# Optimization experiments

Hardware: AMD Instinct MI355X
Metric: run time of the kernel (lower is better)

Reference implementation:

```python
import jax, jax.numpy as jnp
import numpy as np
import math

B, S, D, H = 4, 2048, 1024, 16
HD = D // H
WINDOW = 86400.0 * 7.0  # 7 days, per create_time_mask(window_size=...)


def setup_inputs() -> dict:
    key = jax.random.key(0)
    ks = jax.random.split(key, 12)
    x = jax.random.normal(ks[0], (B, S, D), dtype=jnp.float32)
    # transaction timestamps: uniform over 30 days, sorted per sequence
    timestamps = jnp.sort(jax.random.uniform(ks[1], (B, S), dtype=jnp.float32) * (86400.0 * 30.0), axis=-1)
    init = 0.02
    Wq = jax.random.normal(ks[2], (D, D), dtype=jnp.float32) * init
    bq = jnp.zeros((D,), dtype=jnp.float32)
    Wk = jax.random.normal(ks[3], (D, D), dtype=jnp.float32) * init
    bk = jnp.zeros((D,), dtype=jnp.float32)
    Wv = jax.random.normal(ks[4], (D, D), dtype=jnp.float32) * init
    bv = jnp.zeros((D,), dtype=jnp.float32)
    Wo = jax.random.normal(ks[5], (D, D), dtype=jnp.float32) * init
    bo = jnp.zeros((D,), dtype=jnp.float32)
    Wc = jax.random.normal(ks[6], (1, D), dtype=jnp.float32) * init
    bc = jnp.zeros((1,), dtype=jnp.float32)
    return {"x": x, "timestamps": timestamps, "Wq": Wq, "bq": bq, "Wk": Wk, "bk": bk,
            "Wv": Wv, "bv": bv, "Wo": Wo, "bo": bo, "Wc": Wc, "bc": bc}


def reference(x, timestamps, Wq, bq, Wk, bk, Wv, bv, Wo, bo, Wc, bc):
    b, s, d = x.shape
    scale = 1.0 / math.sqrt(HD)
    # projections (torch Linear: y = x @ W.T + b), split heads -> [b, s, H, HD]
    Q = (x @ Wq.T + bq).reshape(b, s, H, HD)
    K = (x @ Wk.T + bk).reshape(b, s, H, HD)
    V = (x @ Wv.T + bv).reshape(b, s, H, HD)
    # scores [b, H, q, k]
    scores = jnp.einsum('bqhd,bkhd->bhqk', Q, K) * scale
    # time-window mask: attend only within +/- WINDOW seconds
    time_mask = jnp.abs(timestamps[:, :, None] - timestamps[:, None, :]) <= WINDOW  # [b, s, s]
    scores = jnp.where(time_mask[:, None, :, :], scores, -jnp.inf)
    attn = jax.nn.softmax(scores, axis=-1)
    attended = jnp.einsum('bhqk,bkhd->bqhd', attn, V).reshape(b, s, d)
    output = attended @ Wo.T + bo
    change_scores = (output @ Wc.T + bc)[..., 0]  # [b, s]
    return output, change_scores
```

## Files before the change

### kernel.cpp

```cpp
#include <hip/hip_runtime.h>
#include <math.h>

#define BB 4
#define SS 2048
#define DD 1024
#define HH 16
#define HDD 64
#define NN (BB*SS)
#define WINDOWF 604800.0f
#define LOG2E 1.44269504088896340736f
#define SCALE2 (0.125f * LOG2E)

typedef __attribute__((ext_vector_type(8))) short bf16x8;
typedef __attribute__((ext_vector_type(4))) short bf16x4;
typedef __attribute__((ext_vector_type(4))) short s16x4;
typedef __attribute__((ext_vector_type(4))) float f32x4;

__device__ __forceinline__ unsigned short f2b(float f) {
    unsigned int x = __float_as_uint(f);
    unsigned int r = x + 0x7FFFu + ((x >> 16) & 1u);
    return (unsigned short)(r >> 16);
}

__device__ __forceinline__ unsigned int cvt_pk_bf16(float lo, float hi) {
    unsigned int r;
    asm("v_cvt_pk_bf16_f32 %0, %1, %2" : "=v"(r) : "v"(lo), "v"(hi));
    return r;
}

__device__ __forceinline__ void gload16(const unsigned short* g, unsigned short* l) {
    __builtin_amdgcn_global_load_lds(
        (const __attribute__((address_space(1))) unsigned int*)g,
        (__attribute__((address_space(3))) unsigned int*)l, 16, 0, 0);
}

__global__ __launch_bounds__(256)
void cvt_band(const float* __restrict__ x,
              const float* __restrict__ Wq, const float* __restrict__ Wk,
              const float* __restrict__ Wv, const float* __restrict__ Wo,
              const float* __restrict__ ts,
              unsigned short* __restrict__ xb,
              unsigned short* __restrict__ Wqb, unsigned short* __restrict__ Wkb,
              unsigned short* __restrict__ Wvb, unsigned short* __restrict__ Wob,
              int* __restrict__ lo, int* __restrict__ hi)
{
    const int g = blockIdx.x;
    const int tid = threadIdx.x;
    if (g < 12288) {
        const float* src; unsigned short* dst; int i;
        if (g < 8192) { src = x; dst = xb; i = g * 1024 + tid * 4; }
        else {
            const int wi = (g - 8192) >> 10;
            src = (wi == 0) ? Wq : (wi == 1) ? Wk : (wi == 2) ? Wv : Wo;
            dst = (wi == 0) ? Wqb : (wi == 1) ? Wkb : (wi == 2) ? Wvb : Wob;
            i = ((g - 8192) & 1023) * 1024 + tid * 4;
        }
        float4 v = *(const float4*)(src + i);
        s16x4 o;
        o[0] = (short)f2b(v.x); o[1] = (short)f2b(v.y);
        o[2] = (short)f2b(v.z); o[3] = (short)f2b(v.w);
        *(s16x4*)(dst + i) = o;
    } else {
        const int idx = (g - 12288) * 256 + tid;
        const int b = idx / SS, q = idx % SS;
        const float* t = ts + (size_t)b * SS;
        float tq = t[q];
        float lot = tq - WINDOWF - 1.0f;
        float hit = tq + WINDOWF + 1.0f;
        int l = 0, r = q;
        while (l < r) { int m = (l + r) >> 1; if (t[m] < lot) l = m + 1; else r = m; }
        lo[idx] = l;
        int l2 = q, r2 = SS - 1;
        while (l2 < r2) { int m = (l2 + r2 + 1) >> 1; if (t[m] > hit) r2 = m - 1; else l2 = m; }
        hi[idx] = l2;
    }
}

template<int OUTMODE>
__global__ __launch_bounds__(256)
void gemm_bf16(const unsigned short* __restrict__ A,
               const unsigned short* __restrict__ Bw,
               const float* __restrict__ bias,
               void* __restrict__ Y, int M, int N, int K, float alpha)
{
    constexpr int BM = 128, BN = 128, BK = 64;
    __shared__ unsigned short As[BM * BK];
    __shared__ unsigned short Bs[BN * BK];

    const int bm = blockIdx.x * BM;
    const int bn = blockIdx.y * BN;
    const int tid = threadIdx.x;
    const int wid = tid >> 6, l = tid & 63;
    const int wm = (wid >> 1) * 64, wn = (wid & 1) * 64;
    const int lr = l & 15, lg = l >> 4;

    const int srow = l >> 3;
    const int schunk = ((l & 7) ^ srow) * 8;

    f32x4 acc[4][4];
#pragma unroll
    for (int i = 0; i < 4; ++i)
#pragma unroll
        for (int j = 0; j < 4; ++j) acc[i][j] = (f32x4){0.f, 0.f, 0.f, 0.f};

    for (int k0 = 0; k0 < K; k0 += BK) {
#pragma unroll
        for (int i = 0; i < 4; ++i) {
            const int r0 = wid * 32 + i * 8;
            gload16(A  + (size_t)(bm + r0 + srow) * K + k0 + schunk, &As[r0 * BK]);
            gload16(Bw + (size_t)(bn + r0 + srow) * K + k0 + schunk, &Bs[r0 * BK]);
        }
        __syncthreads();

#pragma unroll
        for (int ks = 0; ks < 2; ++ks) {
            bf16x8 af[4], bf[4];
#pragma unroll
            for (int am = 0; am < 4; ++am) {
                const int row = wm + am * 16 + lr;
                af[am] = *(const bf16x8*)&As[row * BK + (((ks * 4 + lg) ^ (row & 7)) * 8)];
            }
#pragma unroll
            for (int nf = 0; nf < 4; ++nf) {
                const int row = wn + nf * 16 + lr;
                bf[nf] = *(const bf16x8*)&Bs[row * BK + (((ks * 4 + lg) ^ (row & 7)) * 8)];
            }
#pragma unroll
            for (int am = 0; am < 4; ++am)
#pragma unroll
                for (int nf = 0; nf < 4; ++nf)
                    acc[am][nf] = __builtin_amdgcn_mfma_f32_16x16x32_bf16(
                        af[am], bf[nf], acc[am][nf], 0, 0, 0);
        }
        __syncthreads();
    }

    float bia[4];
#pragma unroll
    for (int nf = 0; nf < 4; ++nf) bia[nf] = bias[bn + wn + nf * 16 + lr];

#pragma unroll
    for (int am = 0; am < 4; ++am)
#pragma unroll
        for (int nf = 0; nf < 4; ++nf) {
            if (OUTMODE == 2) {
                int mbase = bm + wm + am * 16 + lg * 4;
                int n = bn + wn + nf * 16 + lr;
                int bidx = mbase >> 11, sidx = mbase & (SS - 1);
                s16x4 o;
#pragma unroll
                for (int r = 0; r < 4; ++r)
                    o[r] = (short)f2b((acc[am][nf][r] + bia[nf]) * alpha);
                *(s16x4*)((unsigned short*)Y +
                          (((size_t)(bidx << 10) + n) << 11) + sidx) = o;
            } else {
#pragma unroll
                for (int r = 0; r < 4; ++r) {
                    float o = (acc[am][nf][r] + bia[nf]) * alpha;
                    size_t m = (size_t)(bm + wm + am * 16 + lg * 4 + r);
                    size_t n = (size_t)(bn + wn + nf * 16 + lr);
                    if (OUTMODE == 1) ((unsigned short*)Y)[m * N + n] = f2b(o);
                    else              ((float*)Y)[m * N + n] = o;
                }
            }
        }
}

__global__ __launch_bounds__(256)
void attn_mfma(const unsigned short* __restrict__ Qb, const unsigned short* __restrict__ Kb,
               const unsigned short* __restrict__ Vt, const float* __restrict__ Tg,
               const int* __restrict__ lo, const int* __restrict__ hi,
               unsigned short* __restrict__ Ab)
{
    __shared__ unsigned short Ks[2][64 * 64];
    __shared__ unsigned short Vs[2][64 * 64];

    const int blk = blockIdx.x;
    const int xcd = blk & 7;
    const int idx = blk >> 3;
    const int bh  = xcd * 8 + (idx >> 5);
    const int qt  = idx & 31;
    const int b = bh >> 4, h = bh & 15;

    const int tid = threadIdx.x;
    const int wid = tid >> 6, l = tid & 63;
    const int lr = l & 15, lg = l >> 4;
    const int q0w = qt * 64 + wid * 16;

    const size_t qrow = (size_t)(b * SS + q0w + lr);
    const bf16x8 qf0 = *(const bf16x8*)(Qb + qrow * DD + h * HDD + lg * 8);
    const bf16x8 qf1 = *(const bf16x8*)(Qb + qrow * DD + h * HDD + 32 + lg * 8);

    const float* tb = Tg + (size_t)b * SS;
    const float tq = tb[q0w + lr];
    const float tq_min = tb[qt * 64];
    const float tq_max = tb[qt * 64 + 63];

    const int t0 = lo[b * SS + qt * 64] >> 6;
    const int t1 = hi[b * SS + qt * 64 + 63] >> 6;

    const unsigned short* Kbh = Kb + (size_t)b * SS * DD + h * HDD;
    const unsigned short* Vth = Vt + ((size_t)(b * 1024 + h * HDD)) * SS;

    const int srow = l >> 3;
    const int schunk = ((l & 7) ^ srow) * 8;

    const unsigned short* kg0 = Kbh + (size_t)(t0 * 64 + wid * 16 + srow) * DD + schunk;
    const unsigned short* kg1 = kg0 + 8 * DD;
    const unsigned short* vg0 = Vth + (size_t)(wid * 16 + srow) * SS + t0 * 64 + schunk;
    const unsigned short* vg1 = vg0 + 8 * SS;

    const int x = lr & 7;
    const int ka_off = lr * 64 + ((lg ^ x) << 3);
    const int w = (lg & 1) * 4;
    const int pvA = lr * 64 + ((((lg >> 1) ^ x)) << 3) + w;
    const int pvB = pvA ^ 16;
    const int pvC = pvA ^ 32;
    const int pvD = pvA ^ 48;

    unsigned short *Kc = &Ks[0][0], *Kn = &Ks[1][0];
    unsigned short *Vc = &Vs[0][0], *Vn = &Vs[1][0];
    unsigned short *KnW = Kn, *VnW = Vn;

    float m_ = -1e30f, l_ = 0.f;
    f32x4 o_[4];
#pragma unroll
    for (int df = 0; df < 4; ++df) o_[df] = (f32x4){0.f, 0.f, 0.f, 0.f};

    gload16(kg0, Kc + wid * 1024);
    gload16(kg1, Kc + wid * 1024 + 512);
    gload16(vg0, Vc + wid * 1024);
    gload16(vg1, Vc + wid * 1024 + 512);
    kg0 += 64 * DD; kg1 += 64 * DD; vg0 += 64; vg1 += 64;
    __syncthreads();

    for (int t = t0; t <= t1; ++t) {
        const int kk0 = t * 64;

        if (t < t1) {
            gload16(kg0, Kn + wid * 1024);
            gload16(kg1, Kn + wid * 1024 + 512);
            gload16(vg0, Vn + wid * 1024);
            gload16(vg1, Vn + wid * 1024 + 512);
            kg0 += 64 * DD; kg1 += 64 * DD; vg0 += 64; vg1 += 64;
        }

        f32x4 s[4];
        __builtin_amdgcn_s_setprio(1);
#pragma unroll
        for (int kf = 0; kf < 4; ++kf) {
            bf16x8 ka0 = *(const bf16x8*)(Kc + kf * 1024 + ka_off);
            bf16x8 ka1 = *(const bf16x8*)(Kc + kf * 1024 + (ka_off ^ 32));
            f32x4 z = (f32x4){0.f, 0.f, 0.f, 0.f};
            z = __builtin_amdgcn_mfma_f32_16x16x32_bf16(ka0, qf0, z, 0, 0, 0);
            z = __builtin_amdgcn_mfma_f32_16x16x32_bf16(ka1, qf1, z, 0, 0, 0);
            s[kf] = z;
        }
        __builtin_amdgcn_s_setprio(0);

        const bool needmask = !((tq_max - tb[kk0] <= WINDOWF - 4.0f) &&
                                (tb[kk0 + 63] - tq_min <= WINDOWF - 4.0f));
        if (needmask) {
#pragma unroll
            for (int kf = 0; kf < 4; ++kf) {
                float4 tk4 = *(const float4*)(tb + kk0 + kf * 16 + lg * 4);
                if (!(fabsf(tq - tk4.x) <= WINDOWF)) s[kf][0] = -INFINITY;
                if (!(fabsf(tq - tk4.y) <= WINDOWF)) s[kf][1] = -INFINITY;
                if (!(fabsf(tq - tk4.z) <= WINDOWF)) s[kf][2] = -INFINITY;
                if (!(fabsf(tq - tk4.w) <= WINDOWF)) s[kf][3] = -INFINITY;
            }
        }

        float mt = s[0][0];
#pragma unroll
        for (int kf = 0; kf < 4; ++kf)
#pragma unroll
            for (int r = 0; r < 4; ++r) mt = fmaxf(mt, s[kf][r]);
        mt = fmaxf(mt, __shfl_xor(mt, 16));
        mt = fmaxf(mt, __shfl_xor(mt, 32));
        if (!__all(mt <= m_ + 8.0f)) {
            const float mn = fmaxf(m_, mt);
            const float f_ = __builtin_amdgcn_exp2f(m_ - mn);
            l_ *= f_;
#pragma unroll
            for (int df = 0; df < 4; ++df)
#pragma unroll
                for (int r = 0; r < 4; ++r) o_[df][r] *= f_;
            m_ = mn;
        }
        float rs = 0.f;
#pragma unroll
        for (int kf = 0; kf < 4; ++kf)
#pragma unroll
            for (int r = 0; r < 4; ++r) {
                float p = __builtin_amdgcn_exp2f(s[kf][r] - m_);
                s[kf][r] = p;
                rs += p;
            }
        rs += __shfl_xor(rs, 16);
        rs += __shfl_xor(rs, 32);
        l_ += rs;

        union { unsigned int u[4]; bf16x8 v; } pb[2];
#pragma unroll
        for (int c = 0; c < 2; ++c) {
            pb[c].u[0] = cvt_pk_bf16(s[2 * c][0],     s[2 * c][1]);
            pb[c].u[1] = cvt_pk_bf16(s[2 * c][2],     s[2 * c][3]);
            pb[c].u[2] = cvt_pk_bf16(s[2 * c + 1][0], s[2 * c + 1][1]);
            pb[c].u[3] = cvt_pk_bf16(s[2 * c + 1][2], s[2 * c + 1][3]);
        }

        __builtin_amdgcn_s_setprio(1);
#pragma unroll
        for (int df = 0; df < 4; ++df) {
            const int base = df * 1024;
            union { bf16x4 hh[2]; bf16x8 v; } va0, va1;
            va0.hh[0] = *(const bf16x4*)(Vc + base + pvA);
            va0.hh[1] = *(const bf16x4*)(Vc + base + pvB);
            va1.hh[0] = *(const bf16x4*)(Vc + base + pvC);
            va1.hh[1] = *(const bf16x4*)(Vc + base + pvD);
            o_[df] = __builtin_amdgcn_mfma_f32_16x16x32_bf16(va0.v, pb[0].v, o_[df], 0, 0, 0);
            o_[df] = __builtin_amdgcn_mfma_f32_16x16x32_bf16(va1.v, pb[1].v, o_[df], 0, 0, 0);
        }
        __builtin_amdgcn_s_setprio(0);

        __syncthreads();
        unsigned short* tk = Kc; Kc = Kn; Kn = tk;
        unsigned short* tv = Vc; Vc = Vn; Vn = tv;
        (void)KnW; (void)VnW;
    }

    const float inv = 1.f / l_;
#pragma unroll
    for (int df = 0; df < 4; ++df) {
        s16x4 o;
#pragma unroll
        for (int r = 0; r < 4; ++r) o[r] = (short)f2b(o_[df][r] * inv);
        *(s16x4*)(Ab + qrow * DD + h * HDD + df * 16 + lg * 4) = o;
    }
}

__global__ __launch_bounds__(256)
void change_kernel(const float* __restrict__ out, const float* __restrict__ Wc,
                   const float* __restrict__ bc, float* __restrict__ cs)
{
    int row = blockIdx.x * 4 + (threadIdx.x >> 6);
    int lane = threadIdx.x & 63;
    const float* o = out + (size_t)row * DD;
    float sum = 0.f;
#pragma unroll
    for (int k = 0; k < DD / 256; ++k) {
        int c = lane * 4 + k * 256;
        float4 v = *(const float4*)(o + c);
        float4 w = *(const float4*)(Wc + c);
        sum += v.x * w.x + v.y * w.y + v.z * w.z + v.w * w.w;
    }
#pragma unroll
    for (int off = 1; off < 64; off <<= 1) sum += __shfl_xor(sum, off);
    if (lane == 0) cs[row] = sum + bc[0];
}

extern "C" void kernel_launch(void* const* d_in, const int* in_sizes, int n_in,
                              void* d_out, int out_size, void* d_ws, size_t ws_size,
                              hipStream_t stream)
{
    (void)in_sizes; (void)n_in; (void)out_size; (void)ws_size;
    const float* x  = (const float*)d_in[0];
    const float* ts = (const float*)d_in[1];
    const float* Wq = (const float*)d_in[2];
    const float* bq = (const float*)d_in[3];
    const float* Wk = (const float*)d_in[4];
    const float* bk = (const float*)d_in[5];
    const float* Wv = (const float*)d_in[6];
    const float* bv = (const float*)d_in[7];
    const float* Wo = (const float*)d_in[8];
    const float* bo = (const float*)d_in[9];
    const float* Wc = (const float*)d_in[10];
    const float* bc = (const float*)d_in[11];

    float* out = (float*)d_out;

    unsigned short* xb  = (unsigned short*)d_ws;
    unsigned short* Qb  = xb  + (size_t)NN * DD;
    unsigned short* Kb2 = Qb  + (size_t)NN * DD;
    unsigned short* Vtb = Kb2 + (size_t)NN * DD;
    unsigned short* Abf = Vtb + (size_t)NN * DD;
    unsigned short* Wqb = Abf + (size_t)NN * DD;
    unsigned short* Wkb = Wqb + (size_t)DD * DD;
    unsigned short* Wvb = Wkb + (size_t)DD * DD;
    unsigned short* Wob = Wvb + (size_t)DD * DD;
    int* lo = (int*)(Wob + (size_t)DD * DD);
    int* hi = lo + NN;

    cvt_band<<<12320, 256, 0, stream>>>(x, Wq, Wk, Wv, Wo, ts,
                                        xb, Wqb, Wkb, Wvb, Wob, lo, hi);

    dim3 g(NN / 128, DD / 128);
    gemm_bf16<1><<<g, 256, 0, stream>>>(xb, Wqb, bq, Qb,  NN, DD, DD, SCALE2);
    gemm_bf16<1><<<g, 256, 0, stream>>>(xb, Wkb, bk, Kb2, NN, DD, DD, 1.0f);
    gemm_bf16<2><<<g, 256, 0, stream>>>(xb, Wvb, bv, Vtb, NN, DD, DD, 1.0f);
    attn_mfma<<<BB * HH * (SS / 64), 256, 0, stream>>>(Qb, Kb2, Vtb, ts, lo, hi, Abf);
    gemm_bf16<0><<<g, 256, 0, stream>>>(Abf, Wob, bo, out, NN, DD, DD, 1.0f);
    change_kernel<<<NN / 4, 256, 0, stream>>>(out, Wc, bc, out + (size_t)NN * DD);
}
```

Before: 195.6 us.

## Fuse Q/K/V projections into one GEMM launch and rotate attention LDS swizzle

Merges the three separate Q, K and V projection GEMM launches into a single kernel whose grid y-dimension selects the weight, bias, output and output layout per segment. This removes two launches and lets the three projections share one wave of blocks over the same input, at the cost of runtime branching on the output mode. In the attention kernel, the XOR-based LDS swizzle is replaced by a rotation (add-mod-8) swizzle for the K and V tiles. The row-max reduction is also rewritten as a shallower tree to shorten the dependency chain.

Result: faster. 190.2 us (-2.8%).

```diff
diff --git a/kernel.cpp b/kernel.cpp
--- a/kernel.cpp
+++ b/kernel.cpp
@@ -76,19 +76,15 @@
     }
 }
 
-template<int OUTMODE>
-__global__ __launch_bounds__(256)
-void gemm_bf16(const unsigned short* __restrict__ A,
+__device__ __forceinline__
+void gemm_body(const unsigned short* __restrict__ A,
                const unsigned short* __restrict__ Bw,
                const float* __restrict__ bias,
-               void* __restrict__ Y, int M, int N, int K, float alpha)
-{
-    constexpr int BM = 128, BN = 128, BK = 64;
-    __shared__ unsigned short As[BM * BK];
-    __shared__ unsigned short Bs[BN * BK];
-
-    const int bm = blockIdx.x * BM;
-    const int bn = blockIdx.y * BN;
+               void* __restrict__ Y, int K, int Nout, float alpha,
+               int outmode, int bm, int bn,
+               unsigned short* As, unsigned short* Bs)
+{
+    constexpr int BK = 64;
     const int tid = threadIdx.x;
     const int wid = tid >> 6, l = tid & 63;
     const int wm = (wid >> 1) * 64, wn = (wid & 1) * 64;
@@ -143,7 +139,7 @@
     for (int am = 0; am < 4; ++am)
 #pragma unroll
         for (int nf = 0; nf < 4; ++nf) {
-            if (OUTMODE == 2) {
+            if (outmode == 2) {
                 int mbase = bm + wm + am * 16 + lg * 4;
                 int n = bn + wn + nf * 16 + lr;
                 int bidx = mbase >> 11, sidx = mbase & (SS - 1);
@@ -159,11 +155,45 @@
                     float o = (acc[am][nf][r] + bia[nf]) * alpha;
                     size_t m = (size_t)(bm + wm + am * 16 + lg * 4 + r);
                     size_t n = (size_t)(bn + wn + nf * 16 + lr);
-                    if (OUTMODE == 1) ((unsigned short*)Y)[m * N + n] = f2b(o);
-                    else              ((float*)Y)[m * N + n] = o;
+                    if (outmode == 1) ((unsigned short*)Y)[m * Nout + n] = f2b(o);
+                    else              ((float*)Y)[m * Nout + n] = o;
                 }
             }
         }
+}
+
+__global__ __launch_bounds__(256)
+void gemm_qkv(const unsigned short* __restrict__ xb,
+              const unsigned short* __restrict__ Wqb,
+              const unsigned short* __restrict__ Wkb,
+              const unsigned short* __restrict__ Wvb,
+              const float* __restrict__ bq, const float* __restrict__ bk,
+              const float* __restrict__ bv,
+              unsigned short* __restrict__ Qb, unsigned short* __restrict__ Kb2,
+              unsigned short* __restrict__ Vtb)
+{
+    __shared__ unsigned short As[128 * 64];
+    __shared__ unsigned short Bs[128 * 64];
+    const int seg = blockIdx.y >> 3;
+    const int bn = (blockIdx.y & 7) * 128;
+    const unsigned short* Bw = (seg == 0) ? Wqb : (seg == 1) ? Wkb : Wvb;
+    const float* bias = (seg == 0) ? bq : (seg == 1) ? bk : bv;
+    void* Y = (seg == 0) ? (void*)Qb : (seg == 1) ? (void*)Kb2 : (void*)Vtb;
+    const float alpha = (seg == 0) ? SCALE2 : 1.0f;
+    const int outmode = (seg == 2) ? 2 : 1;
+    gemm_body(xb, Bw, bias, Y, DD, DD, alpha, outmode,
+              blockIdx.x * 128, bn, As, Bs);
+}
+
+__global__ __launch_bounds__(256)
+void gemm_wo(const unsigned short* __restrict__ Abf,
+             const unsigned short* __restrict__ Wob,
+             const float* __restrict__ bo, float* __restrict__ out)
+{
+    __shared__ unsigned short As[128 * 64];
+    __shared__ unsigned short Bs[128 * 64];
+    gemm_body(Abf, Wob, bo, out, DD, DD, 1.0f, 0,
+              blockIdx.x * 128, blockIdx.y * 128, As, Bs);
 }
 
 __global__ __launch_bounds__(256)
@@ -203,24 +233,22 @@
     const unsigned short* Vth = Vt + ((size_t)(b * 1024 + h * HDD)) * SS;
 
     const int srow = l >> 3;
-    const int schunk = ((l & 7) ^ srow) * 8;
+    const int schunk = (((l & 7) - srow) & 7) * 8;
 
     const unsigned short* kg0 = Kbh + (size_t)(t0 * 64 + wid * 16 + srow) * DD + schunk;
     const unsigned short* kg1 = kg0 + 8 * DD;
     const unsigned short* vg0 = Vth + (size_t)(wid * 16 + srow) * SS + t0 * 64 + schunk;
     const unsigned short* vg1 = vg0 + 8 * SS;
 
-    const int x = lr & 7;
-    const int ka_off = lr * 64 + ((lg ^ x) << 3);
-    const int w = (lg & 1) * 4;
-    const int pvA = lr * 64 + ((((lg >> 1) ^ x)) << 3) + w;
-    const int pvB = pvA ^ 16;
-    const int pvC = pvA ^ 32;
-    const int pvD = pvA ^ 48;
+    const int ka_off = lr * 64 + (((lg + lr) & 7) << 3);
+    const int c0 = lg >> 1, h4 = (lg & 1) * 4;
+    const int pv0 = lr * 64 + (((c0 + 0 + lr) & 7) << 3) + h4;
+    const int pv1 = lr * 64 + (((c0 + 2 + lr) & 7) << 3) + h4;
+    const int pv2 = lr * 64 + (((c0 + 4 + lr) & 7) << 3) + h4;
+    const int pv3 = lr * 64 + (((c0 + 6 + lr) & 7) << 3) + h4;
 
     unsigned short *Kc = &Ks[0][0], *Kn = &Ks[1][0];
     unsigned short *Vc = &Vs[0][0], *Vn = &Vs[1][0];
-    unsigned short *KnW = Kn, *VnW = Vn;
 
     float m_ = -1e30f, l_ = 0.f;
     f32x4 o_[4];
@@ -271,11 +299,13 @@
             }
         }
 
-        float mt = s[0][0];
-#pragma unroll
-        for (int kf = 0; kf < 4; ++kf)
-#pragma unroll
-            for (int r = 0; r < 4; ++r) mt = fmaxf(mt, s[kf][r]);
+        float t1_ = fmaxf(fmaxf(s[0][0], s[0][1]), s[0][2]);
+        float t2_ = fmaxf(fmaxf(s[0][3], s[1][0]), s[1][1]);
+        float t3_ = fmaxf(fmaxf(s[1][2], s[1][3]), s[2][0]);
+        float t4_ = fmaxf(fmaxf(s[2][1], s[2][2]), s[2][3]);
+        float t5_ = fmaxf(fmaxf(s[3][0], s[3][1]), s[3][2]);
+        float mt = fmaxf(fmaxf(fmaxf(t1_, t2_), fmaxf(t3_, t4_)),
+                         fmaxf(t5_, s[3][3]));
         mt = fmaxf(mt, __shfl_xor(mt, 16));
         mt = fmaxf(mt, __shfl_xor(mt, 32));
         if (!__all(mt <= m_ + 8.0f)) {
@@ -315,10 +345,10 @@
         for (int df = 0; df < 4; ++df) {
             const int base = df * 1024;
             union { bf16x4 hh[2]; bf16x8 v; } va0, va1;
-            va0.hh[0] = *(const bf16x4*)(Vc + base + pvA);
-            va0.hh[1] = *(const bf16x4*)(Vc + base + pvB);
-            va1.hh[0] = *(const bf16x4*)(Vc + base + pvC);
-            va1.hh[1] = *(const bf16x4*)(Vc + base + pvD);
+            va0.hh[0] = *(const bf16x4*)(Vc + base + pv0);
+            va0.hh[1] = *(const bf16x4*)(Vc + base + pv1);
+            va1.hh[0] = *(const bf16x4*)(Vc + base + pv2);
+            va1.hh[1] = *(const bf16x4*)(Vc + base + pv3);
             o_[df] = __builtin_amdgcn_mfma_f32_16x16x32_bf16(va0.v, pb[0].v, o_[df], 0, 0, 0);
             o_[df] = __builtin_amdgcn_mfma_f32_16x16x32_bf16(va1.v, pb[1].v, o_[df], 0, 0, 0);
         }
@@ -327,7 +357,6 @@
         __syncthreads();
         unsigned short* tk = Kc; Kc = Kn; Kn = tk;
         unsigned short* tv = Vc; Vc = Vn; Vn = tv;
-        (void)KnW; (void)VnW;
     }
 
     const float inv = 1.f / l_;
@@ -395,11 +424,10 @@
     cvt_band<<<12320, 256, 0, stream>>>(x, Wq, Wk, Wv, Wo, ts,
                                         xb, Wqb, Wkb, Wvb, Wob, lo, hi);
 
-    dim3 g(NN / 128, DD / 128);
-    gemm_bf16<1><<<g, 256, 0, stream>>>(xb, Wqb, bq, Qb,  NN, DD, DD, SCALE2);
-    gemm_bf16<1><<<g, 256, 0, stream>>>(xb, Wkb, bk, Kb2, NN, DD, DD, 1.0f);
-    gemm_bf16<2><<<g, 256, 0, stream>>>(xb, Wvb, bv, Vtb, NN, DD, DD, 1.0f);
+    gemm_qkv<<<dim3(NN / 128, 24), 256, 0, stream>>>(
+        xb, Wqb, Wkb, Wvb, bq, bk, bv, Qb, Kb2, Vtb);
+
     attn_mfma<<<BB * HH * (SS / 64), 256, 0, stream>>>(Qb, Kb2, Vtb, ts, lo, hi, Abf);
-    gemm_bf16<0><<<g, 256, 0, stream>>>(Abf, Wob, bo, out, NN, DD, DD, 1.0f);
+    gemm_wo<<<dim3(NN / 128, DD / 128), 256, 0, stream>>>(Abf, Wob, bo, out);
     change_kernel<<<NN / 4, 256, 0, stream>>>(out, Wc, bc, out + (size_t)NN * DD);
 }
```
